# Optimization experiments

Hardware: AMD Instinct MI355X
Metric: run time of the kernel (lower is better)

## Reference

```python
import jax, jax.numpy as jnp
import numpy as np


def setup_inputs() -> dict:
    key = jax.random.key(0)
    k1, k2 = jax.random.split(key)
    B, S, D = 8, 2048, 128
    x = jax.random.normal(k1, (B, S, D), dtype=jnp.float32)
    y = jax.random.normal(k2, (B, S, D), dtype=jnp.float32)
    return {"x": x, "y": y}


def reference(x, y):
    # m1 = x @ y^T  -> [B, Sx, Sy]; unscaled dot-product attention
    m1 = jnp.einsum('bsd,btd->bst', x, y)
    n1 = jax.nn.softmax(m1, axis=-1)
    o1 = jnp.einsum('bst,btd->bsd', n1, y)   # [B, Sx, D]
    a1 = o1 * x                               # gating multiply

    # symmetric pass: m2 = y @ x^T (== m1 transposed)
    m2 = jnp.einsum('btd,bsd->bts', y, x)
    n2 = jax.nn.softmax(m2, axis=-1)
    o2 = jnp.einsum('bts,bsd->btd', n2, x)   # [B, Sy, D]
    a2 = o2 * y

    return jnp.concatenate([a1, a2], axis=-1)  # [B, S, 2D]
```

## Files before the change

### kernel.cpp

```cpp
#include <hip/hip_runtime.h>
#include <hip/hip_bf16.h>

typedef __attribute__((ext_vector_type(8))) short bf16x8;
typedef __attribute__((ext_vector_type(8))) _Float16 f16x8;
typedef __attribute__((ext_vector_type(4))) float f32x4;
typedef __attribute__((ext_vector_type(16))) float f32x16;

#define MFMA16B(a, b, c) __builtin_amdgcn_mfma_f32_16x16x32_bf16(a, b, c, 0, 0, 0)
#define MFMA32F(a, b, c) __builtin_amdgcn_mfma_f32_32x32x16_f16(a, b, c, 0, 0, 0)

static constexpr int S = 2048;
static constexpr int D = 128;

__device__ inline unsigned short f2b(float f) {
    union { float f; unsigned int u; } v; v.f = f;
    unsigned int u = v.u;
    return (unsigned short)((u + 0x7FFFu + ((u >> 16) & 1u)) >> 16);
}
__device__ inline float b2f(unsigned short h) {
    union { unsigned int u; float f; } v; v.u = ((unsigned int)h) << 16;
    return v.f;
}
__device__ inline unsigned int pack2(float a, float b) {
    return (unsigned int)f2b(a) | ((unsigned int)f2b(b) << 16);
}
__device__ inline unsigned int pkh(float a, float b) {
    union { _Float16 h; unsigned short u; } ua, ub;
    ua.h = (_Float16)a; ub.h = (_Float16)b;
    return (unsigned int)ua.u | ((unsigned int)ub.u << 16);
}

__device__ __forceinline__ void gload16(const void* g, void* l) {
    __builtin_amdgcn_global_load_lds(
        (const __attribute__((address_space(1))) unsigned int*)(unsigned long long)(g),
        (__attribute__((address_space(3))) unsigned int*)(unsigned int)(unsigned long long)(l),
        16, 0, 0);
}

__global__ __launch_bounds__(256) void bimodal_prep5(
    const float* __restrict__ X, const float* __restrict__ Y,
    unsigned short* __restrict__ WS)
{
    const int bid = blockIdx.x;
    const int t = bid & 63;
    const int b = (bid >> 6) & 7;
    const int mat = bid >> 9;
    const float* src = mat ? Y : X;
    char* kf = (char*)(WS + (size_t)(mat * 2 + 0) * (8ull * S * D)) + (size_t)(b * 64 + t) * 8192;
    char* vt = (char*)(WS + (size_t)(mat * 2 + 1) * (8ull * S * D)) + (size_t)(b * 64 + t) * 8192;

    __shared__ float ftile[32][129];
    const int tid = threadIdx.x;
    const float* tsrc = src + ((size_t)(b * S + t * 32)) * D;
#pragma unroll
    for (int it = 0; it < 4; ++it) {
        int idx = tid + it * 256;
        int row = idx >> 5, ch = idx & 31;
        float4 v = *(const float4*)(tsrc + (size_t)row * D + ch * 4);
        ftile[row][ch * 4 + 0] = v.x; ftile[row][ch * 4 + 1] = v.y;
        ftile[row][ch * 4 + 2] = v.z; ftile[row][ch * 4 + 3] = v.w;
    }
    __syncthreads();
#pragma unroll
    for (int it = 0; it < 8; ++it) {
        int w = tid + it * 256;
        int row = w >> 6, cp = w & 63;
        unsigned int d = pkh(ftile[row][2 * cp], ftile[row][2 * cp + 1]);
        int byte = (row * 256 + cp * 4) ^ ((row & 7) << 4);
        *(unsigned int*)(kf + byte) = d;
    }
#pragma unroll
    for (int it = 0; it < 8; ++it) {
        int w = tid + it * 256;
        int dd = w >> 4, jp = w & 15;
        unsigned int d = pkh(ftile[2 * jp][dd], ftile[2 * jp + 1][dd]);
        int byte = (dd * 64 + jp * 4) ^ ((dd & 7) << 4);
        *(unsigned int*)(vt + byte) = d;
    }
}

__global__ __launch_bounds__(256) void bimodal_attn_v6(
    const float* __restrict__ X, const float* __restrict__ Y,
    const unsigned short* __restrict__ WS, float* __restrict__ Out)
{
    const int orig = blockIdx.x;
    const int wg = (orig & 7) * 64 + (orig >> 3);
    const int qt = wg & 31;
    const int p  = (wg >> 5) & 1;
    const int b  = wg >> 6;

    const float* Q = p ? Y : X;
    const int kvmat = p ? 0 : 1;
    const int ocol = p * D;

    __shared__ __align__(16) char smem[65536];

    const int tid = threadIdx.x;
    const int wv = tid >> 6;
    const int lane = tid & 63;
    const int qp = lane & 31;
    const int h = lane >> 5;
    const int grp = wv >> 1;
    const int qb = wv & 1;
    const int i0 = qt * 64 + qb * 32;

    const float* qrow = Q + ((size_t)(b * S + i0 + qp)) * D;
    f16x8 qf[8];
#pragma unroll
    for (int kc = 0; kc < 8; ++kc) {
        const float* qpp = qrow + kc * 16 + h * 8;
        float4 f0 = *(const float4*)qpp;
        float4 f1 = *(const float4*)(qpp + 4);
        f16x8 tq;
        tq[0] = (_Float16)f0.x; tq[1] = (_Float16)f0.y; tq[2] = (_Float16)f0.z; tq[3] = (_Float16)f0.w;
        tq[4] = (_Float16)f1.x; tq[5] = (_Float16)f1.y; tq[6] = (_Float16)f1.z; tq[7] = (_Float16)f1.w;
        qf[kc] = tq;
    }

    f32x16 o[4];
#pragma unroll
    for (int db = 0; db < 4; ++db)
#pragma unroll
        for (int i = 0; i < 16; ++i) o[db][i] = 0.f;
    float m = -1e30f, l = 0.f;

    const char* kfb = (const char*)(WS + (size_t)(kvmat * 2 + 0) * (8ull * S * D)) + (size_t)b * (S * D * 2);
    const char* vtb = (const char*)(WS + (size_t)(kvmat * 2 + 1) * (8ull * S * D)) + (size_t)b * (S * D * 2);
    const int gl = qb * 64 + lane;
    char* mybase = smem + grp * 32768;

    auto stage = [&](int t, int bi) {
        char* kb = mybase + bi * 16384;
        char* vb = kb + 8192;
        const char* kt = kfb + t * 8192;
        const char* vp = vtb + t * 8192;
#pragma unroll
        for (int i = 0; i < 4; ++i)
            gload16(kt + gl * 16 + i * 2048, kb + gl * 16 + i * 2048);
#pragma unroll
        for (int i = 0; i < 4; ++i)
            gload16(vp + gl * 16 + i * 2048, vb + gl * 16 + i * 2048);
    };

    stage(grp, 0);
    __syncthreads();

    for (int s = 0; s < 32; ++s) {
        if (s < 31) stage(2 * (s + 1) + grp, (s + 1) & 1);
        const char* kb = mybase + (s & 1) * 16384;
        const char* vb = kb + 8192;

        f32x16 sT;
#pragma unroll
        for (int i = 0; i < 16; ++i) sT[i] = 0.f;
        __builtin_amdgcn_s_setprio(1);
#pragma unroll
        for (int kc = 0; kc < 8; ++kc) {
            int byte = (qp * 256 + kc * 32 + h * 16) ^ ((qp & 7) << 4);
            f16x8 kA = *(const f16x8*)(kb + byte);
            sT = MFMA32F(kA, qf[kc], sT);
        }
        __builtin_amdgcn_s_setprio(0);

        float pmax = sT[0];
#pragma unroll
        for (int i = 1; i < 16; ++i) pmax = fmaxf(pmax, sT[i]);
        pmax = fmaxf(pmax, __shfl_xor(pmax, 32));
        if (!__all(pmax - m <= 8.f)) {
            float mn = fmaxf(m, pmax);
            float alpha = __expf(m - mn);
            m = mn; l *= alpha;
#pragma unroll
            for (int db = 0; db < 4; ++db)
#pragma unroll
                for (int i = 0; i < 16; ++i) o[db][i] *= alpha;
        }
        float rs = 0.f;
#pragma unroll
        for (int i = 0; i < 16; ++i) { sT[i] = __expf(sT[i] - m); rs += sT[i]; }
        rs += __shfl_xor(rs, 32);
        l += rs;

        unsigned w8[8];
#pragma unroll
        for (int t2 = 0; t2 < 4; ++t2) {
            w8[2 * t2]     = pkh(sT[4 * t2 + 0], sT[4 * t2 + 1]);
            w8[2 * t2 + 1] = pkh(sT[4 * t2 + 2], sT[4 * t2 + 3]);
        }
        union { unsigned u[4]; f16x8 v; } bf0, bf1;
#pragma unroll
        for (int v2 = 0; v2 < 2; ++v2) {
            unsigned a0 = w8[v2], b0 = w8[2 + v2];
            asm volatile("v_permlane32_swap_b32 %0, %1" : "+v"(a0), "+v"(b0));
            bf0.u[v2] = a0; bf0.u[2 + v2] = b0;
            unsigned a1 = w8[4 + v2], b1 = w8[6 + v2];
            asm volatile("v_permlane32_swap_b32 %0, %1" : "+v"(a1), "+v"(b1));
            bf1.u[v2] = a1; bf1.u[2 + v2] = b1;
        }

        __builtin_amdgcn_s_setprio(1);
#pragma unroll
        for (int db = 0; db < 4; ++db) {
            int rowbyte = (db * 32 + qp) * 64;
            int x0 = (rowbyte + h * 16) ^ ((qp & 7) << 4);
            int x1 = (rowbyte + 32 + h * 16) ^ ((qp & 7) << 4);
            f16x8 v0 = *(const f16x8*)(vb + x0);
            f16x8 v1 = *(const f16x8*)(vb + x1);
            o[db] = MFMA32F(v0, bf0.v, o[db]);
            o[db] = MFMA32F(v1, bf1.v, o[db]);
        }
        __builtin_amdgcn_s_setprio(0);

        __syncthreads();
    }

    {
        float2* mlp = (float2*)(smem + wv * 512);
        mlp[lane] = make_float2(m, l);
    }
    __syncthreads();
    float2 pml = ((float2*)(smem + (wv ^ 2) * 512))[lane];
    float mstar = fmaxf(m, pml.x);
    float sc = __expf(m - mstar);
    float lstar = sc * l + __expf(pml.x - mstar) * pml.y;
#pragma unroll
    for (int db = 0; db < 4; ++db)
#pragma unroll
        for (int i = 0; i < 16; ++i) o[db][i] *= sc;
    __syncthreads();

    float* ob = (float*)(smem + 4096);
#pragma unroll
    for (int db = 0; db < 4; ++db) {
        if (grp == 1) {
#pragma unroll
            for (int i = 0; i < 16; ++i) ob[qb * 1024 + i * 64 + lane] = o[db][i];
        }
        __syncthreads();
        if (grp == 0) {
#pragma unroll
            for (int i = 0; i < 16; ++i) o[db][i] += ob[qb * 1024 + i * 64 + lane];
        }
        __syncthreads();
    }

    if (grp == 0) {
        const float invl = 1.f / lstar;
        float* outr = Out + ((size_t)(b * S + i0 + qp)) * (2 * D) + ocol;
#pragma unroll
        for (int db = 0; db < 4; ++db)
#pragma unroll
            for (int t2 = 0; t2 < 4; ++t2) {
                int d0 = db * 32 + t2 * 8 + h * 4;
                float4 qv = *(const float4*)(qrow + d0);
                float4 ov;
                ov.x = o[db][4 * t2 + 0] * invl * qv.x;
                ov.y = o[db][4 * t2 + 1] * invl * qv.y;
                ov.z = o[db][4 * t2 + 2] * invl * qv.z;
                ov.w = o[db][4 * t2 + 3] * invl * qv.w;
                *(float4*)(outr + d0) = ov;
            }
    }
}

__global__ __launch_bounds__(256) void bimodal_attn_fb(
    const float* __restrict__ X, const float* __restrict__ Y,
    float* __restrict__ Out)
{
    const int bid = blockIdx.x;
    const int qt = bid & 31;
    const int p  = (bid >> 5) & 1;
    const int b  = bid >> 6;

    const float* Q  = p ? Y : X;
    const float* KV = p ? X : Y;
    const int ocol = p * D;

    __shared__ unsigned short Khi[64 * D];
    __shared__ unsigned short Klo[64 * D];
    __shared__ unsigned short Vt[D * 64];
    __shared__ unsigned short Psh[4][16 * 72];

    const int tid = threadIdx.x;
    const int wv = tid >> 6;
    const int lane = tid & 63;
    const int c = lane & 15;
    const int g = lane >> 4;
    const int i0 = qt * 64 + wv * 16;

    const float* qbase = Q + ((size_t)(b * S + i0 + c)) * D;
    bf16x8 qhi[4], qlo[4];
#pragma unroll
    for (int kc = 0; kc < 4; ++kc) {
        const float* qp = qbase + kc * 32 + g * 8;
        float4 f0 = *(const float4*)qp;
        float4 f1 = *(const float4*)(qp + 4);
        float fv[8] = {f0.x, f0.y, f0.z, f0.w, f1.x, f1.y, f1.z, f1.w};
        bf16x8 th, tl;
#pragma unroll
        for (int i = 0; i < 8; ++i) {
            unsigned short hh = f2b(fv[i]);
            th[i] = (short)hh;
            tl[i] = (short)f2b(fv[i] - b2f(hh));
        }
        qhi[kc] = th; qlo[kc] = tl;
    }

    f32x4 o[8];
#pragma unroll
    for (int nb = 0; nb < 8; ++nb) { o[nb][0] = 0.f; o[nb][1] = 0.f; o[nb][2] = 0.f; o[nb][3] = 0.f; }
    float m[4], l[4];
#pragma unroll
    for (int r = 0; r < 4; ++r) { m[r] = -1e30f; l[r] = 0.f; }

    const float* kvb = KV + (size_t)b * S * D;
    unsigned short* pbuf = Psh[wv];

    for (int j0 = 0; j0 < S; j0 += 64) {
#pragma unroll
        for (int t = 0; t < 4; ++t) {
            int task = tid + t * 256;
            int jr = task >> 4, sl = task & 15;
            const float* src = kvb + (size_t)(j0 + jr) * D + sl * 8;
            float4 f0 = *(const float4*)src;
            float4 f1 = *(const float4*)(src + 4);
            float fv[8] = {f0.x, f0.y, f0.z, f0.w, f1.x, f1.y, f1.z, f1.w};
            unsigned short hv[8];
            float lv[8];
#pragma unroll
            for (int i = 0; i < 8; ++i) {
                hv[i] = f2b(fv[i]);
                lv[i] = fv[i] - b2f(hv[i]);
            }
            uint4 wh, wl;
            wh.x = (unsigned int)hv[0] | ((unsigned int)hv[1] << 16);
            wh.y = (unsigned int)hv[2] | ((unsigned int)hv[3] << 16);
            wh.z = (unsigned int)hv[4] | ((unsigned int)hv[5] << 16);
            wh.w = (unsigned int)hv[6] | ((unsigned int)hv[7] << 16);
            wl.x = pack2(lv[0], lv[1]); wl.y = pack2(lv[2], lv[3]);
            wl.z = pack2(lv[4], lv[5]); wl.w = pack2(lv[6], lv[7]);
            int byte = (jr * 256 + sl * 16) ^ ((jr & 7) << 4);
            *(uint4*)((char*)Khi + byte) = wh;
            *(uint4*)((char*)Klo + byte) = wl;
        }
#pragma unroll
        for (int t = 0; t < 2; ++t) {
            int task = tid + t * 256;
            int jp = task & 31, dc = task >> 5;
            const float* s0 = kvb + (size_t)(j0 + 2 * jp) * D + dc * 8;
            const float* s1 = s0 + D;
            float4 a0 = *(const float4*)s0, a1 = *(const float4*)(s0 + 4);
            float4 b0 = *(const float4*)s1, b1 = *(const float4*)(s1 + 4);
            float av[8] = {a0.x, a0.y, a0.z, a0.w, a1.x, a1.y, a1.z, a1.w};
            float bv[8] = {b0.x, b0.y, b0.z, b0.w, b1.x, b1.y, b1.z, b1.w};
#pragma unroll
            for (int i = 0; i < 8; ++i) {
                int d = dc * 8 + i;
                int byte = (d * 128 + jp * 4) ^ ((d & 7) << 4);
                *(unsigned int*)((char*)Vt + byte) = pack2(av[i], bv[i]);
            }
        }
        __syncthreads();

        f32x4 sF[4];
#pragma unroll
        for (int nb = 0; nb < 4; ++nb) {
            f32x4 acc; acc[0] = 0.f; acc[1] = 0.f; acc[2] = 0.f; acc[3] = 0.f;
#pragma unroll
            for (int kc = 0; kc < 4; ++kc) {
                int row = nb * 16 + c;
                int byte = (row * 256 + (kc * 32 + g * 8) * 2) ^ ((row & 7) << 4);
                bf16x8 kh = *(const bf16x8*)((char*)Khi + byte);
                bf16x8 kl = *(const bf16x8*)((char*)Klo + byte);
                acc = MFMA16B(qhi[kc], kh, acc);
                acc = MFMA16B(qhi[kc], kl, acc);
                acc = MFMA16B(qlo[kc], kh, acc);
            }
            sF[nb] = acc;
        }

#pragma unroll
        for (int r = 0; r < 4; ++r) {
            float v = fmaxf(fmaxf(sF[0][r], sF[1][r]), fmaxf(sF[2][r], sF[3][r]));
            v = fmaxf(v, __shfl_xor(v, 1));
            v = fmaxf(v, __shfl_xor(v, 2));
            v = fmaxf(v, __shfl_xor(v, 4));
            v = fmaxf(v, __shfl_xor(v, 8));
            float mn = fmaxf(m[r], v);
            float alpha = __expf(m[r] - mn);
            m[r] = mn;
            float rs = 0.f;
#pragma unroll
            for (int nb = 0; nb < 4; ++nb) {
                float pv = __expf(sF[nb][r] - mn);
                sF[nb][r] = pv;
                rs += pv;
            }
            rs += __shfl_xor(rs, 1);
            rs += __shfl_xor(rs, 2);
            rs += __shfl_xor(rs, 4);
            rs += __shfl_xor(rs, 8);
            l[r] = l[r] * alpha + rs;
#pragma unroll
            for (int nb = 0; nb < 8; ++nb) o[nb][r] *= alpha;
        }

#pragma unroll
        for (int nb = 0; nb < 4; ++nb)
#pragma unroll
            for (int r = 0; r < 4; ++r)
                pbuf[(g * 4 + r) * 72 + nb * 16 + c] = f2b(sF[nb][r]);

        bf16x8 pa[2];
#pragma unroll
        for (int kc = 0; kc < 2; ++kc)
            pa[kc] = *(const bf16x8*)(pbuf + c * 72 + kc * 32 + g * 8);

#pragma unroll
        for (int nb = 0; nb < 8; ++nb) {
#pragma unroll
            for (int kc = 0; kc < 2; ++kc) {
                int d = nb * 16 + c;
                int byte = (d * 128 + (kc * 32 + g * 8) * 2) ^ ((d & 7) << 4);
                bf16x8 vf = *(const bf16x8*)((char*)Vt + byte);
                o[nb] = MFMA16B(pa[kc], vf, o[nb]);
            }
        }
        __syncthreads();
    }

    float* outb = Out + ((size_t)(b * S + i0)) * (2 * D) + ocol;
    const float* qg = Q + (size_t)(b * S + i0) * D;
#pragma unroll
    for (int r = 0; r < 4; ++r) {
        int row = g * 4 + r;
        float inv = 1.f / l[r];
#pragma unroll
        for (int nb = 0; nb < 8; ++nb) {
            int col = nb * 16 + c;
            float qv = qg[(size_t)row * D + col];
            outb[(size_t)row * (2 * D) + col] = o[nb][r] * inv * qv;
        }
    }
}

extern "C" void kernel_launch(void* const* d_in, const int* in_sizes, int n_in,
                              void* d_out, int out_size, void* d_ws, size_t ws_size,
                              hipStream_t stream) {
    const float* x = (const float*)d_in[0];
    const float* y = (const float*)d_in[1];
    float* out = (float*)d_out;
    const size_t need = 4ull * 8 * S * D * 2;
    if (ws_size >= need) {
        hipLaunchKernelGGL(bimodal_prep5, dim3(1024), dim3(256), 0, stream,
                           x, y, (unsigned short*)d_ws);
        hipLaunchKernelGGL(bimodal_attn_v6, dim3(512), dim3(256), 0, stream,
                           x, y, (const unsigned short*)d_ws, out);
    } else {
        hipLaunchKernelGGL(bimodal_attn_fb, dim3(512), dim3(256), 0, stream, x, y, out);
    }
}
```

Before: 74.47 us.

## Double query rows per wave and split KV four ways with 512-thread blocks

Each wave now processes two 32-row query tiles against every staged K/V tile, so each LDS read of K and V feeds twice as many MFMAs. The block grows to 512 threads covering 128 query rows, with the KV sequence split into four 512-key ranges handled by separate wave groups. Partial softmax states are merged through a two-level shared-memory reduction. The grid halves to 256 blocks and LDS grows to 128KB with higher register pressure per wave, which risks lower occupancy and leaving CUs idle.

```diff
diff --git a/kernel.cpp b/kernel.cpp
--- a/kernel.cpp
+++ b/kernel.cpp
@@ -79,89 +79,74 @@
     }
 }
 
-__global__ __launch_bounds__(256) void bimodal_attn_v6(
+__global__ __launch_bounds__(512) void bimodal_attn_v9(
     const float* __restrict__ X, const float* __restrict__ Y,
     const unsigned short* __restrict__ WS, float* __restrict__ Out)
 {
     const int orig = blockIdx.x;
-    const int wg = (orig & 7) * 64 + (orig >> 3);
-    const int qt = wg & 31;
-    const int p  = (wg >> 5) & 1;
-    const int b  = wg >> 6;
+    const int wg = (orig & 7) * 32 + (orig >> 3);
+    const int qt = wg & 15;
+    const int p  = (wg >> 4) & 1;
+    const int b  = wg >> 5;
 
     const float* Q = p ? Y : X;
     const int kvmat = p ? 0 : 1;
     const int ocol = p * D;
 
-    __shared__ __align__(16) char smem[65536];
+    __shared__ __align__(16) char smem[131072];
 
     const int tid = threadIdx.x;
     const int wv = tid >> 6;
     const int lane = tid & 63;
     const int qp = lane & 31;
     const int h = lane >> 5;
-    const int grp = wv >> 1;
-    const int qb = wv & 1;
-    const int i0 = qt * 64 + qb * 32;
-
-    const float* qrow = Q + ((size_t)(b * S + i0 + qp)) * D;
-    f16x8 qf[8];
+    const int s = wv & 1;
+    const int g = wv >> 1;
+    const int i0 = qt * 128 + s * 64;
+
+    const float* qrow0 = Q + ((size_t)(b * S + i0 + qp)) * D;
+    const float* qrow1 = qrow0 + 32 * D;
+    f16x8 qf0[8], qf1[8];
 #pragma unroll
     for (int kc = 0; kc < 8; ++kc) {
-        const float* qpp = qrow + kc * 16 + h * 8;
-        float4 f0 = *(const float4*)qpp;
-        float4 f1 = *(const float4*)(qpp + 4);
-        f16x8 tq;
-        tq[0] = (_Float16)f0.x; tq[1] = (_Float16)f0.y; tq[2] = (_Float16)f0.z; tq[3] = (_Float16)f0.w;
-        tq[4] = (_Float16)f1.x; tq[5] = (_Float16)f1.y; tq[6] = (_Float16)f1.z; tq[7] = (_Float16)f1.w;
-        qf[kc] = tq;
-    }
-
-    f32x16 o[4];
+        const float* q0 = qrow0 + kc * 16 + h * 8;
+        const float* q1 = qrow1 + kc * 16 + h * 8;
+        float4 a0 = *(const float4*)q0, a1 = *(const float4*)(q0 + 4);
+        float4 c0 = *(const float4*)q1, c1 = *(const float4*)(q1 + 4);
+        f16x8 t0, t1;
+        t0[0] = (_Float16)a0.x; t0[1] = (_Float16)a0.y; t0[2] = (_Float16)a0.z; t0[3] = (_Float16)a0.w;
+        t0[4] = (_Float16)a1.x; t0[5] = (_Float16)a1.y; t0[6] = (_Float16)a1.z; t0[7] = (_Float16)a1.w;
+        t1[0] = (_Float16)c0.x; t1[1] = (_Float16)c0.y; t1[2] = (_Float16)c0.z; t1[3] = (_Float16)c0.w;
+        t1[4] = (_Float16)c1.x; t1[5] = (_Float16)c1.y; t1[6] = (_Float16)c1.z; t1[7] = (_Float16)c1.w;
+        qf0[kc] = t0; qf1[kc] = t1;
+    }
+
+    f32x16 o0[4], o1[4];
 #pragma unroll
     for (int db = 0; db < 4; ++db)
 #pragma unroll
-        for (int i = 0; i < 16; ++i) o[db][i] = 0.f;
-    float m = -1e30f, l = 0.f;
+        for (int i = 0; i < 16; ++i) { o0[db][i] = 0.f; o1[db][i] = 0.f; }
+    float m0 = -1e30f, l0 = 0.f, m1 = -1e30f, l1 = 0.f;
 
     const char* kfb = (const char*)(WS + (size_t)(kvmat * 2 + 0) * (8ull * S * D)) + (size_t)b * (S * D * 2);
     const char* vtb = (const char*)(WS + (size_t)(kvmat * 2 + 1) * (8ull * S * D)) + (size_t)b * (S * D * 2);
-    const int gl = qb * 64 + lane;
-    char* mybase = smem + grp * 32768;
+    const int gl = s * 64 + lane;
+    char* mybase = smem + g * 32768;
 
     auto stage = [&](int t, int bi) {
         char* kb = mybase + bi * 16384;
-        char* vb = kb + 8192;
-        const char* kt = kfb + t * 8192;
-        const char* vp = vtb + t * 8192;
+        const char* kt = kfb + (size_t)(g * 16 + t) * 8192;
+        const char* vp = vtb + (size_t)(g * 16 + t) * 8192;
 #pragma unroll
         for (int i = 0; i < 4; ++i)
             gload16(kt + gl * 16 + i * 2048, kb + gl * 16 + i * 2048);
 #pragma unroll
         for (int i = 0; i < 4; ++i)
-            gload16(vp + gl * 16 + i * 2048, vb + gl * 16 + i * 2048);
+            gload16(vp + gl * 16 + i * 2048, kb + 8192 + gl * 16 + i * 2048);
     };
 
-    stage(grp, 0);
-    __syncthreads();
-
-    for (int s = 0; s < 32; ++s) {
-        if (s < 31) stage(2 * (s + 1) + grp, (s + 1) & 1);
-        const char* kb = mybase + (s & 1) * 16384;
-        const char* vb = kb + 8192;
-
-        f32x16 sT;
-#pragma unroll
-        for (int i = 0; i < 16; ++i) sT[i] = 0.f;
-        __builtin_amdgcn_s_setprio(1);
-#pragma unroll
-        for (int kc = 0; kc < 8; ++kc) {
-            int byte = (qp * 256 + kc * 32 + h * 16) ^ ((qp & 7) << 4);
-            f16x8 kA = *(const f16x8*)(kb + byte);
-            sT = MFMA32F(kA, qf[kc], sT);
-        }
-        __builtin_amdgcn_s_setprio(0);
-
+    auto softmax_pack = [&](f32x16& sT, float& m, float& l, f32x16 (&o)[4],
+                            f16x8& pb0, f16x8& pb1) {
         float pmax = sT[0];
 #pragma unroll
         for (int i = 1; i < 16; ++i) pmax = fmaxf(pmax, sT[i]);
@@ -197,6 +182,33 @@
             asm volatile("v_permlane32_swap_b32 %0, %1" : "+v"(a1), "+v"(b1));
             bf1.u[v2] = a1; bf1.u[2 + v2] = b1;
         }
+        pb0 = bf0.v; pb1 = bf1.v;
+    };
+
+    stage(0, 0);
+    __syncthreads();
+
+    for (int t = 0; t < 16; ++t) {
+        if (t < 15) stage(t + 1, (t + 1) & 1);
+        const char* kb = mybase + (t & 1) * 16384;
+        const char* vb = kb + 8192;
+
+        f32x16 sT0, sT1;
+#pragma unroll
+        for (int i = 0; i < 16; ++i) { sT0[i] = 0.f; sT1[i] = 0.f; }
+        __builtin_amdgcn_s_setprio(1);
+#pragma unroll
+        for (int kc = 0; kc < 8; ++kc) {
+            int byte = (qp * 256 + kc * 32 + h * 16) ^ ((qp & 7) << 4);
+            f16x8 kA = *(const f16x8*)(kb + byte);
+            sT0 = MFMA32F(kA, qf0[kc], sT0);
+            sT1 = MFMA32F(kA, qf1[kc], sT1);
+        }
+        __builtin_amdgcn_s_setprio(0);
+
+        f16x8 p00, p01, p10, p11;
+        softmax_pack(sT0, m0, l0, o0, p00, p01);
+        softmax_pack(sT1, m1, l1, o1, p10, p11);
 
         __builtin_amdgcn_s_setprio(1);
 #pragma unroll
@@ -206,59 +218,119 @@
             int x1 = (rowbyte + 32 + h * 16) ^ ((qp & 7) << 4);
             f16x8 v0 = *(const f16x8*)(vb + x0);
             f16x8 v1 = *(const f16x8*)(vb + x1);
-            o[db] = MFMA32F(v0, bf0.v, o[db]);
-            o[db] = MFMA32F(v1, bf1.v, o[db]);
+            o0[db] = MFMA32F(v0, p00, o0[db]);
+            o0[db] = MFMA32F(v1, p01, o0[db]);
+            o1[db] = MFMA32F(v0, p10, o1[db]);
+            o1[db] = MFMA32F(v1, p11, o1[db]);
         }
         __builtin_amdgcn_s_setprio(0);
 
         __syncthreads();
     }
 
-    {
-        float2* mlp = (float2*)(smem + wv * 512);
-        mlp[lane] = make_float2(m, l);
-    }
-    __syncthreads();
-    float2 pml = ((float2*)(smem + (wv ^ 2) * 512))[lane];
-    float mstar = fmaxf(m, pml.x);
-    float sc = __expf(m - mstar);
-    float lstar = sc * l + __expf(pml.x - mstar) * pml.y;
+    float4* mls = (float4*)smem;
+    mls[wv * 64 + lane] = make_float4(m0, l0, m1, l1);
+    __syncthreads();
+    float4 q2 = mls[(wv ^ 2) * 64 + lane];
+    float4 q4 = mls[(wv ^ 4) * 64 + lane];
+    float4 q6 = mls[(wv ^ 6) * 64 + lane];
+    float ms0 = fmaxf(fmaxf(m0, q2.x), fmaxf(q4.x, q6.x));
+    float ls0 = __expf(m0 - ms0) * l0 + __expf(q2.x - ms0) * q2.y
+              + __expf(q4.x - ms0) * q4.y + __expf(q6.x - ms0) * q6.y;
+    float sc0 = __expf(m0 - ms0);
+    float ms1 = fmaxf(fmaxf(m1, q2.z), fmaxf(q4.z, q6.z));
+    float ls1 = __expf(m1 - ms1) * l1 + __expf(q2.z - ms1) * q2.w
+              + __expf(q4.z - ms1) * q4.w + __expf(q6.z - ms1) * q6.w;
+    float sc1 = __expf(m1 - ms1);
 #pragma unroll
     for (int db = 0; db < 4; ++db)
 #pragma unroll
-        for (int i = 0; i < 16; ++i) o[db][i] *= sc;
-    __syncthreads();
-
-    float* ob = (float*)(smem + 4096);
-#pragma unroll
-    for (int db = 0; db < 4; ++db) {
-        if (grp == 1) {
-#pragma unroll
-            for (int i = 0; i < 16; ++i) ob[qb * 1024 + i * 64 + lane] = o[db][i];
-        }
-        __syncthreads();
-        if (grp == 0) {
-#pragma unroll
-            for (int i = 0; i < 16; ++i) o[db][i] += ob[qb * 1024 + i * 64 + lane];
-        }
-        __syncthreads();
-    }
-
-    if (grp == 0) {
-        const float invl = 1.f / lstar;
-        float* outr = Out + ((size_t)(b * S + i0 + qp)) * (2 * D) + ocol;
+        for (int i = 0; i < 16; ++i) { o0[db][i] *= sc0; o1[db][i] *= sc1; }
+    __syncthreads();
+
+    const int r = s + 2 * (g >> 1);
+    float* rg = (float*)(smem + r * 32768);
+    if (g & 1) {
+#pragma unroll
+        for (int db = 0; db < 4; ++db)
+#pragma unroll
+            for (int t2 = 0; t2 < 4; ++t2) {
+                *(float4*)(rg + ((db * 4 + t2) * 64 + lane) * 4) =
+                    make_float4(o0[db][4*t2+0], o0[db][4*t2+1], o0[db][4*t2+2], o0[db][4*t2+3]);
+                *(float4*)(rg + (((4 + db) * 4 + t2) * 64 + lane) * 4) =
+                    make_float4(o1[db][4*t2+0], o1[db][4*t2+1], o1[db][4*t2+2], o1[db][4*t2+3]);
+            }
+    }
+    __syncthreads();
+    if (!(g & 1)) {
+#pragma unroll
+        for (int db = 0; db < 4; ++db)
+#pragma unroll
+            for (int t2 = 0; t2 < 4; ++t2) {
+                float4 a = *(const float4*)(rg + ((db * 4 + t2) * 64 + lane) * 4);
+                o0[db][4*t2+0] += a.x; o0[db][4*t2+1] += a.y;
+                o0[db][4*t2+2] += a.z; o0[db][4*t2+3] += a.w;
+                float4 c = *(const float4*)(rg + (((4 + db) * 4 + t2) * 64 + lane) * 4);
+                o1[db][4*t2+0] += c.x; o1[db][4*t2+1] += c.y;
+                o1[db][4*t2+2] += c.z; o1[db][4*t2+3] += c.w;
+            }
+    }
+    __syncthreads();
+    float* rb = (float*)(smem + s * 32768);
+    if (g == 2) {
+#pragma unroll
+        for (int db = 0; db < 4; ++db)
+#pragma unroll
+            for (int t2 = 0; t2 < 4; ++t2) {
+                *(float4*)(rb + ((db * 4 + t2) * 64 + lane) * 4) =
+                    make_float4(o0[db][4*t2+0], o0[db][4*t2+1], o0[db][4*t2+2], o0[db][4*t2+3]);
+                *(float4*)(rb + (((4 + db) * 4 + t2) * 64 + lane) * 4) =
+                    make_float4(o1[db][4*t2+0], o1[db][4*t2+1], o1[db][4*t2+2], o1[db][4*t2+3]);
+            }
+    }
+    __syncthreads();
+
+    if (g == 0) {
+#pragma unroll
+        for (int db = 0; db < 4; ++db)
+#pragma unroll
+            for (int t2 = 0; t2 < 4; ++t2) {
+                float4 a = *(const float4*)(rb + ((db * 4 + t2) * 64 + lane) * 4);
+                o0[db][4*t2+0] += a.x; o0[db][4*t2+1] += a.y;
+                o0[db][4*t2+2] += a.z; o0[db][4*t2+3] += a.w;
+                float4 c = *(const float4*)(rb + (((4 + db) * 4 + t2) * 64 + lane) * 4);
+                o1[db][4*t2+0] += c.x; o1[db][4*t2+1] += c.y;
+                o1[db][4*t2+2] += c.z; o1[db][4*t2+3] += c.w;
+            }
+        const float inv0 = 1.f / ls0;
+        float* outr0 = Out + ((size_t)(b * S + i0 + qp)) * (2 * D) + ocol;
 #pragma unroll
         for (int db = 0; db < 4; ++db)
 #pragma unroll
             for (int t2 = 0; t2 < 4; ++t2) {
                 int d0 = db * 32 + t2 * 8 + h * 4;
-                float4 qv = *(const float4*)(qrow + d0);
+                float4 qv = *(const float4*)(qrow0 + d0);
                 float4 ov;
-                ov.x = o[db][4 * t2 + 0] * invl * qv.x;
-                ov.y = o[db][4 * t2 + 1] * invl * qv.y;
-                ov.z = o[db][4 * t2 + 2] * invl * qv.z;
-                ov.w = o[db][4 * t2 + 3] * invl * qv.w;
-                *(float4*)(outr + d0) = ov;
+                ov.x = o0[db][4*t2+0] * inv0 * qv.x;
+                ov.y = o0[db][4*t2+1] * inv0 * qv.y;
+                ov.z = o0[db][4*t2+2] * inv0 * qv.z;
+                ov.w = o0[db][4*t2+3] * inv0 * qv.w;
+                *(float4*)(outr0 + d0) = ov;
+            }
+        const float inv1 = 1.f / ls1;
+        float* outr1 = Out + ((size_t)(b * S + i0 + 32 + qp)) * (2 * D) + ocol;
+#pragma unroll
+        for (int db = 0; db < 4; ++db)
+#pragma unroll
+            for (int t2 = 0; t2 < 4; ++t2) {
+                int d0 = db * 32 + t2 * 8 + h * 4;
+                float4 qv = *(const float4*)(qrow1 + d0);
+                float4 ov;
+                ov.x = o1[db][4*t2+0] * inv1 * qv.x;
+                ov.y = o1[db][4*t2+1] * inv1 * qv.y;
+                ov.z = o1[db][4*t2+2] * inv1 * qv.z;
+                ov.w = o1[db][4*t2+3] * inv1 * qv.w;
+                *(float4*)(outr1 + d0) = ov;
             }
     }
 }
@@ -454,7 +526,7 @@
     if (ws_size >= need) {
         hipLaunchKernelGGL(bimodal_prep5, dim3(1024), dim3(256), 0, stream,
                            x, y, (unsigned short*)d_ws);
-        hipLaunchKernelGGL(bimodal_attn_v6, dim3(512), dim3(256), 0, stream,
+        hipLaunchKernelGGL(bimodal_attn_v9, dim3(256), dim3(512), 0, stream,
                            x, y, (const unsigned short*)d_ws, out);
     } else {
         hipLaunchKernelGGL(bimodal_attn_fb, dim3(512), dim3(256), 0, stream, x, y, out);
```

After: 67.43 us. 1.1x faster.

## Split KV sequence across four wave groups with 512-thread blocks, drop double buffering

Applied to the files above, without the earlier changes.

The attention kernel now uses 512 threads per block. Four wave-pair groups each process a disjoint quarter of the KV tiles (16 tiles each) instead of two groups interleaving 32 tiles. Double-buffered LDS staging is replaced by single-buffer staging per group with syncs around each tile, and the final softmax merge combines four partial (m, l, O) states through a two-level LDS reduction. This increases waves per block and shortens the serial KV loop. In exchange, the next tile's loads no longer overlap with compute, and the cross-group reduction costs more.

```diff
diff --git a/kernel.cpp b/kernel.cpp
--- a/kernel.cpp
+++ b/kernel.cpp
@@ -79,7 +79,7 @@
     }
 }
 
-__global__ __launch_bounds__(256) void bimodal_attn_v6(
+__global__ __launch_bounds__(512, 4) void bimodal_attn_v13(
     const float* __restrict__ X, const float* __restrict__ Y,
     const unsigned short* __restrict__ WS, float* __restrict__ Out)
 {
@@ -100,9 +100,9 @@
     const int lane = tid & 63;
     const int qp = lane & 31;
     const int h = lane >> 5;
-    const int grp = wv >> 1;
-    const int qb = wv & 1;
-    const int i0 = qt * 64 + qb * 32;
+    const int s = wv & 1;
+    const int g = wv >> 1;
+    const int i0 = qt * 64 + s * 32;
 
     const float* qrow = Q + ((size_t)(b * S + i0 + qp)) * D;
     f16x8 qf[8];
@@ -126,14 +126,13 @@
 
     const char* kfb = (const char*)(WS + (size_t)(kvmat * 2 + 0) * (8ull * S * D)) + (size_t)b * (S * D * 2);
     const char* vtb = (const char*)(WS + (size_t)(kvmat * 2 + 1) * (8ull * S * D)) + (size_t)b * (S * D * 2);
-    const int gl = qb * 64 + lane;
-    char* mybase = smem + grp * 32768;
-
-    auto stage = [&](int t, int bi) {
-        char* kb = mybase + bi * 16384;
-        char* vb = kb + 8192;
-        const char* kt = kfb + t * 8192;
-        const char* vp = vtb + t * 8192;
+    const int gl = s * 64 + lane;
+    char* kb = smem + g * 16384;
+    char* vb = kb + 8192;
+
+    auto stage = [&](int t) {
+        const char* kt = kfb + (size_t)(g * 16 + t) * 8192;
+        const char* vp = vtb + (size_t)(g * 16 + t) * 8192;
 #pragma unroll
         for (int i = 0; i < 4; ++i)
             gload16(kt + gl * 16 + i * 2048, kb + gl * 16 + i * 2048);
@@ -142,13 +141,10 @@
             gload16(vp + gl * 16 + i * 2048, vb + gl * 16 + i * 2048);
     };
 
-    stage(grp, 0);
-    __syncthreads();
-
-    for (int s = 0; s < 32; ++s) {
-        if (s < 31) stage(2 * (s + 1) + grp, (s + 1) & 1);
-        const char* kb = mybase + (s & 1) * 16384;
-        const char* vb = kb + 8192;
+    stage(0);
+
+    for (int t = 0; t < 16; ++t) {
+        __syncthreads();
 
         f32x16 sT;
 #pragma unroll
@@ -212,39 +208,67 @@
         __builtin_amdgcn_s_setprio(0);
 
         __syncthreads();
-    }
-
-    {
-        float2* mlp = (float2*)(smem + wv * 512);
-        mlp[lane] = make_float2(m, l);
-    }
-    __syncthreads();
-    float2 pml = ((float2*)(smem + (wv ^ 2) * 512))[lane];
-    float mstar = fmaxf(m, pml.x);
+        if (t < 15) stage(t + 1);
+    }
+
+    float2* mls = (float2*)smem;
+    mls[wv * 64 + lane] = make_float2(m, l);
+    __syncthreads();
+    float2 q2 = mls[(wv ^ 2) * 64 + lane];
+    float2 q4 = mls[(wv ^ 4) * 64 + lane];
+    float2 q6 = mls[(wv ^ 6) * 64 + lane];
+    float mstar = fmaxf(fmaxf(m, q2.x), fmaxf(q4.x, q6.x));
+    float lstar = __expf(m - mstar) * l + __expf(q2.x - mstar) * q2.y
+                + __expf(q4.x - mstar) * q4.y + __expf(q6.x - mstar) * q6.y;
     float sc = __expf(m - mstar);
-    float lstar = sc * l + __expf(pml.x - mstar) * pml.y;
 #pragma unroll
     for (int db = 0; db < 4; ++db)
 #pragma unroll
         for (int i = 0; i < 16; ++i) o[db][i] *= sc;
     __syncthreads();
 
-    float* ob = (float*)(smem + 4096);
-#pragma unroll
-    for (int db = 0; db < 4; ++db) {
-        if (grp == 1) {
-#pragma unroll
-            for (int i = 0; i < 16; ++i) ob[qb * 1024 + i * 64 + lane] = o[db][i];
-        }
-        __syncthreads();
-        if (grp == 0) {
-#pragma unroll
-            for (int i = 0; i < 16; ++i) o[db][i] += ob[qb * 1024 + i * 64 + lane];
-        }
-        __syncthreads();
-    }
-
-    if (grp == 0) {
+    const int r = s + 2 * (g & 1);
+    float* rg = (float*)(smem + r * 16384);
+    if (g >= 2) {
+#pragma unroll
+        for (int db = 0; db < 4; ++db)
+#pragma unroll
+            for (int t2 = 0; t2 < 4; ++t2)
+                *(float4*)(rg + ((db * 4 + t2) * 64 + lane) * 4) =
+                    make_float4(o[db][4*t2+0], o[db][4*t2+1], o[db][4*t2+2], o[db][4*t2+3]);
+    }
+    __syncthreads();
+    if (g < 2) {
+#pragma unroll
+        for (int db = 0; db < 4; ++db)
+#pragma unroll
+            for (int t2 = 0; t2 < 4; ++t2) {
+                float4 a = *(const float4*)(rg + ((db * 4 + t2) * 64 + lane) * 4);
+                o[db][4*t2+0] += a.x; o[db][4*t2+1] += a.y;
+                o[db][4*t2+2] += a.z; o[db][4*t2+3] += a.w;
+            }
+    }
+    __syncthreads();
+    float* rb = (float*)(smem + s * 16384);
+    if (g == 1) {
+#pragma unroll
+        for (int db = 0; db < 4; ++db)
+#pragma unroll
+            for (int t2 = 0; t2 < 4; ++t2)
+                *(float4*)(rb + ((db * 4 + t2) * 64 + lane) * 4) =
+                    make_float4(o[db][4*t2+0], o[db][4*t2+1], o[db][4*t2+2], o[db][4*t2+3]);
+    }
+    __syncthreads();
+
+    if (g == 0) {
+#pragma unroll
+        for (int db = 0; db < 4; ++db)
+#pragma unroll
+            for (int t2 = 0; t2 < 4; ++t2) {
+                float4 a = *(const float4*)(rb + ((db * 4 + t2) * 64 + lane) * 4);
+                o[db][4*t2+0] += a.x; o[db][4*t2+1] += a.y;
+                o[db][4*t2+2] += a.z; o[db][4*t2+3] += a.w;
+            }
         const float invl = 1.f / lstar;
         float* outr = Out + ((size_t)(b * S + i0 + qp)) * (2 * D) + ocol;
 #pragma unroll
@@ -454,7 +478,7 @@
     if (ws_size >= need) {
         hipLaunchKernelGGL(bimodal_prep5, dim3(1024), dim3(256), 0, stream,
                            x, y, (unsigned short*)d_ws);
-        hipLaunchKernelGGL(bimodal_attn_v6, dim3(512), dim3(256), 0, stream,
+        hipLaunchKernelGGL(bimodal_attn_v13, dim3(512), dim3(512), 0, stream,
                            x, y, (const unsigned short*)d_ws, out);
     } else {
         hipLaunchKernelGGL(bimodal_attn_fb, dim3(512), dim3(256), 0, stream, x, y, out);
```

New measurement: 86.16 us. +15.7%, slower.
